# Kernel tuning notes

Measured on AMD Instinct MI355X. Metric: run time of the kernel, lower is better.

The kernel has to match this reference:

```python
import jax, jax.numpy as jnp
import numpy as np

K = 8
HID = 32
BOUND = 5.0
SIGMA_MIN = 1e-4
MIN_DERIV = 1e-3
B, T, C = 32, 4096, 512


def setup_inputs() -> dict:
    key = jax.random.key(0)
    k1, k2, k3 = jax.random.split(key, 3)
    x = jax.random.normal(k1, (B, T, C), jnp.float32)
    W1 = jax.random.normal(k2, (HID, 2), jnp.float32) * 0.5
    b1 = jnp.zeros((HID,), jnp.float32)
    W2 = jax.random.normal(k3, (3 * K + 1, HID), jnp.float32) * 0.1
    b2 = jnp.zeros((3 * K + 1,), jnp.float32)
    return {"x": x, "W1": W1, "b1": b1, "W2": W2, "b2": b2}


def _rqs_forward(x2d, kx, ky, d):
    # x2d: (BC, T); kx, ky, d: (BC, K+1)
    w = kx[:, 1:] - kx[:, :-1]
    h = ky[:, 1:] - ky[:, :-1]
    s = h / jnp.maximum(w, 1e-8)
    idx = jax.vmap(lambda a, v: jnp.searchsorted(a, v, side='right'))(kx, x2d) - 1
    idx = jnp.clip(idx, 0, K - 1)  # (BC, T)
    g = lambda t, i: jnp.take_along_axis(t, i, axis=1)
    w_k = g(w, idx)
    h_k = g(h, idx)
    s_k = g(s, idx)
    d_k = g(d, idx)
    d_k1 = g(d, jnp.minimum(idx + 1, K))
    kx_l = g(kx, idx)
    ky_l = g(ky, idx)
    zeta = jnp.clip((x2d - kx_l) / jnp.maximum(w_k, 1e-8), 0.0, 1.0)
    numer = h_k * (s_k * zeta * zeta + d_k * zeta * (1.0 - zeta))
    denom = s_k + (d_k1 + d_k - 2.0 * s_k) * zeta * (1.0 - zeta)
    z2d = ky_l + numer / jnp.maximum(denom, 1e-8)
    tail = (x2d < -BOUND) | (x2d > BOUND)
    return jnp.where(tail, x2d, z2d)


def reference(x, W1, b1, W2, b2):
    Bb, Tt, Cc = x.shape
    # affine standardisation (unbiased std matching torch.std default)
    mu = jnp.mean(x, axis=1, keepdims=True)
    sig = jnp.maximum(jnp.std(x, axis=1, ddof=1, keepdims=True), SIGMA_MIN)
    z_pre = (x - mu) / sig  # (B, T, C)
    zd = jax.lax.stop_gradient(z_pre)
    skew = jnp.mean(zd ** 3, axis=1)          # (B, C)
    ekurt = jnp.mean(zd ** 4, axis=1) - 3.0   # (B, C)
    stats = jnp.stack([skew, ekurt], axis=-1).reshape(Bb * Cc, 2)
    hid = jax.nn.relu(stats @ W1.T + b1)
    raw = hid @ W2.T + b2                      # (BC, 3K+1)
    widths = jax.nn.softmax(raw[:, :K], axis=-1) * (2.0 * BOUND)
    heights = jax.nn.softmax(raw[:, K:2 * K], axis=-1) * (2.0 * BOUND)
    derivs = jax.nn.softplus(raw[:, 2 * K:]) + MIN_DERIV  # (BC, K+1)
    pad = jnp.full((widths.shape[0], 1), -BOUND, widths.dtype)
    kx = jnp.concatenate([pad, -BOUND + jnp.cumsum(widths, axis=-1)], axis=-1)
    ky = jnp.concatenate([pad, -BOUND + jnp.cumsum(heights, axis=-1)], axis=-1)
    x2d = jnp.transpose(z_pre, (0, 2, 1)).reshape(Bb * Cc, Tt)
    z2d = _rqs_forward(x2d, kx, ky, derivs)
    return jnp.transpose(z2d.reshape(Bb, Cc, Tt), (0, 2, 1))
```

## Files before the change

kernel.cpp:

```cpp
#include <hip/hip_runtime.h>
#include <math.h>

#define KNOTS 8
#define HIDN 32
#define TT 4096
#define CC 512
#define NB 32
#define BOUNDF 5.0f
#define CT 32
#define NTG 16
#define TPT (TT / NTG)
#define NPAIR (TPT / 2)

__global__ __launch_bounds__(512, 2)
void k_fused(const float* __restrict__ x, const float* __restrict__ W1,
             const float* __restrict__ b1, const float* __restrict__ W2,
             const float* __restrict__ b2, float* __restrict__ out)
{
    const int bb = blockIdx.y;
    const int c0 = blockIdx.x * CT;
    const int ci = threadIdx.x & (CT - 1);
    const int tg = threadIdx.x >> 5;

    __shared__ float red[NTG][4][CT];
    __shared__ float mom[4][CT];
    __shared__ float pA[CT], pB[CT];
    __shared__ float pKx[7][CT];
    __shared__ float2 bZ[KNOTS][CT];
    __shared__ float2 bY[KNOTS][CT];
    __shared__ float2 bD[KNOTS][CT];

    const size_t base = (size_t)bb * TT * CC + c0 + ci;
    const float* pxt = x + base + (size_t)tg * CC;

    unsigned int xp[NPAIR];
    float s1 = 0.f, s2 = 0.f, s3 = 0.f, s4 = 0.f;
    #pragma unroll
    for (int m = 0; m < NPAIR; ++m) {
        const float v0 = pxt[(size_t)(2*m)     * (NTG * CC)];
        const float v1 = pxt[(size_t)(2*m + 1) * (NTG * CC)];
        const float v0sq = v0 * v0, v1sq = v1 * v1;
        s1 += v0;                    s1 += v1;
        s2 = fmaf(v0,   v0,   s2);   s2 = fmaf(v1,   v1,   s2);
        s3 = fmaf(v0sq, v0,   s3);   s3 = fmaf(v1sq, v1,   s3);
        s4 = fmaf(v0sq, v0sq, s4);   s4 = fmaf(v1sq, v1sq, s4);
        unsigned int pk;
        asm("v_cvt_pk_bf16_f32 %0, %1, %2" : "=v"(pk) : "v"(v0), "v"(v1));
        xp[m] = pk;
    }
    red[tg][0][ci] = s1; red[tg][1][ci] = s2;
    red[tg][2][ci] = s3; red[tg][3][ci] = s4;
    __syncthreads();

    if (threadIdx.x < 4 * CT) {
        const int m = threadIdx.x >> 5, c = threadIdx.x & (CT - 1);
        float acc = 0.f;
        #pragma unroll
        for (int g = 0; g < NTG; ++g) acc += red[g][m][c];
        mom[m][c] = acc;
    }
    __syncthreads();

    if (threadIdx.x < CT) {
        const int c = threadIdx.x;
        const float n  = (float)TT;
        const float t1 = mom[0][c], t2 = mom[1][c], t3 = mom[2][c], t4 = mom[3][c];
        const float mu  = t1 / n;
        const float ex2 = t2 / n, ex3 = t3 / n, ex4 = t4 / n;
        float var = (t2 - n * mu * mu) / (n - 1.f);
        var = fmaxf(var, 0.f);
        const float sig  = fmaxf(sqrtf(var), 1e-4f);
        const float inv  = 1.f / sig;
        const float mu2  = mu * mu;
        const float ez3  = ex3 - 3.f * mu * ex2 + 2.f * mu * mu2;
        const float ez4  = ex4 - 4.f * mu * ex3 + 6.f * mu2 * ex2 - 3.f * mu2 * mu2;
        const float inv2 = inv * inv;
        const float skew  = ez3 * inv2 * inv;
        const float ekurt = ez4 * inv2 * inv2 - 3.f;

        float hid[HIDN];
        #pragma unroll
        for (int h = 0; h < HIDN; ++h) {
            float v = fmaf(W1[2*h], skew, fmaf(W1[2*h+1], ekurt, b1[h]));
            hid[h] = fmaxf(v, 0.f);
        }

        float e[KNOTS], kxr[KNOTS+1], kyr[KNOTS+1], dr[KNOTS+1];
        {
            float mx = -1e30f;
            #pragma unroll
            for (int o = 0; o < KNOTS; ++o) {
                float acc = b2[o];
                #pragma unroll
                for (int h = 0; h < HIDN; ++h) acc = fmaf(W2[o*HIDN + h], hid[h], acc);
                e[o] = acc; mx = fmaxf(mx, acc);
            }
            float sum = 0.f;
            #pragma unroll
            for (int o = 0; o < KNOTS; ++o) { e[o] = expf(e[o] - mx); sum += e[o]; }
            const float scale = (2.f * BOUNDF) / sum;
            float cum = -BOUNDF; kxr[0] = -BOUNDF;
            #pragma unroll
            for (int o = 0; o < KNOTS; ++o) { cum = fmaf(e[o], scale, cum); kxr[o+1] = cum; }
        }
        {
            float mx = -1e30f;
            #pragma unroll
            for (int o = 0; o < KNOTS; ++o) {
                float acc = b2[KNOTS + o];
                #pragma unroll
                for (int h = 0; h < HIDN; ++h) acc = fmaf(W2[(KNOTS+o)*HIDN + h], hid[h], acc);
                e[o] = acc; mx = fmaxf(mx, acc);
            }
            float sum = 0.f;
            #pragma unroll
            for (int o = 0; o < KNOTS; ++o) { e[o] = expf(e[o] - mx); sum += e[o]; }
            const float scale = (2.f * BOUNDF) / sum;
            float cum = -BOUNDF; kyr[0] = -BOUNDF;
            #pragma unroll
            for (int o = 0; o < KNOTS; ++o) { cum = fmaf(e[o], scale, cum); kyr[o+1] = cum; }
        }
        #pragma unroll
        for (int o = 0; o < KNOTS+1; ++o) {
            float acc = b2[2*KNOTS + o];
            #pragma unroll
            for (int h = 0; h < HIDN; ++h) acc = fmaf(W2[(2*KNOTS+o)*HIDN + h], hid[h], acc);
            float sp = fmaxf(acc, 0.f) + log1pf(expf(-fabsf(acc)));
            dr[o] = sp + 1e-3f;
        }

        pA[c] = inv;
        pB[c] = -mu * inv;
        #pragma unroll
        for (int j = 1; j <= 7; ++j) pKx[j-1][c] = kxr[j];
        #pragma unroll
        for (int j = 0; j < KNOTS; ++j) {
            const float w    = kxr[j+1] - kxr[j];
            const float wm   = fmaxf(w, 1e-8f);
            const float invw = 1.f / wm;
            const float h    = kyr[j+1] - kyr[j];
            bZ[j][c] = make_float2(-kxr[j] * invw, invw);
            bY[j][c] = make_float2(kyr[j], h);
            bD[j][c] = make_float2(dr[j], dr[j] + dr[j+1]);
        }
    }
    __syncthreads();

    const float a  = pA[ci];
    const float bz = pB[ci];
    const float kx1 = pKx[0][ci], kx2 = pKx[1][ci], kx3 = pKx[2][ci],
                kx4 = pKx[3][ci], kx5 = pKx[4][ci], kx6 = pKx[5][ci],
                kx7 = pKx[6][ci];
    float* pot = out + base + (size_t)tg * CC;

    #pragma unroll
    for (int m = 0; m < NPAIR; ++m) {
        const unsigned int u = xp[m];
        const float xv0 = __uint_as_float(u << 16);
        const float xv1 = __uint_as_float(u & 0xffff0000u);
        #pragma unroll
        for (int j = 0; j < 2; ++j) {
            const float xv = (j == 0) ? xv0 : xv1;
            const float z = fmaf(xv, a, bz);
            const bool  c4 = z >= kx4;
            const float mB = c4 ? kx6 : kx2;
            const bool  cB = z >= mB;
            const float nLo = c4 ? kx5 : kx1;
            const float nHi = c4 ? kx7 : kx3;
            const float mC = cB ? nHi : nLo;
            const bool  cC = z >= mC;
            const int off = (c4 ? 4*CT : 0) + (cB ? 2*CT : 0) + (cC ? CT : 0) + ci;

            const float2 Z = ((const float2*)bZ)[off];
            const float2 Y = ((const float2*)bY)[off];
            const float2 D = ((const float2*)bD)[off];

            const float zeta = fmaf(z, Z.y, Z.x);
            const float uu   = fmaf(-zeta, zeta, zeta);
            const float s    = Y.y * Z.y;
            const float R    = fmaf(-2.f, s, D.y);
            const float den  = fmaf(R, uu, s);
            const float inner= fmaf(s * zeta, zeta, D.x * uu);
            const float res  = fmaf(Y.y * inner,
                                    __builtin_amdgcn_rcpf(fmaxf(den, 1e-8f)), Y.x);
            const float o = (fabsf(z) > BOUNDF) ? z : res;
            __builtin_nontemporal_store(o, &pot[(size_t)(2*m + j) * (NTG * CC)]);
        }
    }
}

extern "C" void kernel_launch(void* const* d_in, const int* in_sizes, int n_in,
                              void* d_out, int out_size, void* d_ws, size_t ws_size,
                              hipStream_t stream) {
    const float* x  = (const float*)d_in[0];
    const float* W1 = (const float*)d_in[1];
    const float* b1 = (const float*)d_in[2];
    const float* W2 = (const float*)d_in[3];
    const float* b2 = (const float*)d_in[4];
    float* out = (float*)d_out;

    k_fused<<<dim3(CC / CT, NB), dim3(512), 0, stream>>>(x, W1, b1, W2, b2, out);
}
```

Before: 121.2 us.

## Cache only half the column in registers, re-read the rest to double occupancy

Each thread now keeps only 128 of its 256 timesteps packed as bf16 in registers, down from all 256. The remaining timesteps are streamed once for the moment sums and then re-read from global memory in reverse order during the transform pass, so the most recently loaded data is likely still in cache. Fewer registers allow the launch bound to rise to 4 blocks per SM, which should improve latency hiding. The cost is reading about half of the input a second time, plus extra loop overhead.

```diff
diff --git a/kernel.cpp b/kernel.cpp
--- a/kernel.cpp
+++ b/kernel.cpp
@@ -10,9 +10,9 @@
 #define CT 32
 #define NTG 16
 #define TPT (TT / NTG)
-#define NPAIR (TPT / 2)
-
-__global__ __launch_bounds__(512, 2)
+#define NHOLD 64
+
+__global__ __launch_bounds__(512, 4)
 void k_fused(const float* __restrict__ x, const float* __restrict__ W1,
              const float* __restrict__ b1, const float* __restrict__ W2,
              const float* __restrict__ b2, float* __restrict__ out)
@@ -33,10 +33,10 @@
     const size_t base = (size_t)bb * TT * CC + c0 + ci;
     const float* pxt = x + base + (size_t)tg * CC;
 
-    unsigned int xp[NPAIR];
+    unsigned int xp[NHOLD];
     float s1 = 0.f, s2 = 0.f, s3 = 0.f, s4 = 0.f;
     #pragma unroll
-    for (int m = 0; m < NPAIR; ++m) {
+    for (int m = 0; m < NHOLD; ++m) {
         const float v0 = pxt[(size_t)(2*m)     * (NTG * CC)];
         const float v1 = pxt[(size_t)(2*m + 1) * (NTG * CC)];
         const float v0sq = v0 * v0, v1sq = v1 * v1;
@@ -47,6 +47,15 @@
         unsigned int pk;
         asm("v_cvt_pk_bf16_f32 %0, %1, %2" : "=v"(pk) : "v"(v0), "v"(v1));
         xp[m] = pk;
+    }
+    #pragma unroll 8
+    for (int k = 2 * NHOLD; k < TPT; ++k) {
+        const float v  = pxt[(size_t)k * (NTG * CC)];
+        const float v2 = v * v;
+        s1 += v;
+        s2 = fmaf(v,  v,  s2);
+        s3 = fmaf(v2, v,  s3);
+        s4 = fmaf(v2, v2, s4);
     }
     red[tg][0][ci] = s1; red[tg][1][ci] = s2;
     red[tg][2][ci] = s3; red[tg][3][ci] = s4;
@@ -153,8 +162,40 @@
                 kx7 = pKx[6][ci];
     float* pot = out + base + (size_t)tg * CC;
 
+    for (int kb = TPT / 8 - 1; kb >= 2 * NHOLD / 8; --kb) {
+        float xv[8];
+        #pragma unroll
+        for (int j = 0; j < 8; ++j)
+            xv[j] = pxt[(size_t)(kb * 8 + j) * (NTG * CC)];
+        #pragma unroll
+        for (int j = 0; j < 8; ++j) {
+            const float z = fmaf(xv[j], a, bz);
+            const bool  c4 = z >= kx4;
+            const float mB = c4 ? kx6 : kx2;
+            const bool  cB = z >= mB;
+            const float nLo = c4 ? kx5 : kx1;
+            const float nHi = c4 ? kx7 : kx3;
+            const float mC = cB ? nHi : nLo;
+            const bool  cC = z >= mC;
+            const int off = (c4 ? 4*CT : 0) + (cB ? 2*CT : 0) + (cC ? CT : 0) + ci;
+            const float2 Z = ((const float2*)bZ)[off];
+            const float2 Y = ((const float2*)bY)[off];
+            const float2 D = ((const float2*)bD)[off];
+            const float zeta = fmaf(z, Z.y, Z.x);
+            const float uu   = fmaf(-zeta, zeta, zeta);
+            const float s    = Y.y * Z.y;
+            const float R    = fmaf(-2.f, s, D.y);
+            const float den  = fmaf(R, uu, s);
+            const float inner= fmaf(s * zeta, zeta, D.x * uu);
+            const float res  = fmaf(Y.y * inner,
+                                    __builtin_amdgcn_rcpf(fmaxf(den, 1e-8f)), Y.x);
+            const float o = (fabsf(z) > BOUNDF) ? z : res;
+            __builtin_nontemporal_store(o, &pot[(size_t)(kb * 8 + j) * (NTG * CC)]);
+        }
+    }
+
     #pragma unroll
-    for (int m = 0; m < NPAIR; ++m) {
+    for (int m = 0; m < NHOLD; ++m) {
         const unsigned int u = xp[m];
         const float xv0 = __uint_as_float(u << 16);
         const float xv1 = __uint_as_float(u & 0xffff0000u);
@@ -170,11 +211,9 @@
             const float mC = cB ? nHi : nLo;
             const bool  cC = z >= mC;
             const int off = (c4 ? 4*CT : 0) + (cB ? 2*CT : 0) + (cC ? CT : 0) + ci;
-
             const float2 Z = ((const float2*)bZ)[off];
             const float2 Y = ((const float2*)bY)[off];
             const float2 D = ((const float2*)bD)[off];
-
             const float zeta = fmaf(z, Z.y, Z.x);
             const float uu   = fmaf(-zeta, zeta, zeta);
             const float s    = Y.y * Z.y;
```

Result: no change. 120.8 us (-0.3%).

## Stream input through double-buffered LDS via async global_load_lds

Applied to the files above, without the earlier changes.

Replaces direct per-thread global loads in the moment-accumulation pass with async global-to-LDS loads into a double-buffered staging area. Each wave issues 16 rows per chunk, waits on vmcnt, and reads values back from LDS while the next chunk is in flight. This aims to keep more memory requests outstanding and cut register pressure from the fully unrolled loads. In exchange it adds 64KB of LDS, which may limit occupancy to fewer than two blocks per CU, and relies on hand-placed waitcnt ordering.

```diff
diff --git a/kernel.cpp b/kernel.cpp
--- a/kernel.cpp
+++ b/kernel.cpp
@@ -11,6 +11,11 @@
 #define NTG 16
 #define TPT (TT / NTG)
 #define NPAIR (TPT / 2)
+#define CH 16
+#define NBUF (TPT / CH)
+
+typedef __attribute__((address_space(3))) void       lds_void;
+typedef const __attribute__((address_space(1))) void g_void;
 
 __global__ __launch_bounds__(512, 2)
 void k_fused(const float* __restrict__ x, const float* __restrict__ W1,
@@ -21,7 +26,10 @@
     const int c0 = blockIdx.x * CT;
     const int ci = threadIdx.x & (CT - 1);
     const int tg = threadIdx.x >> 5;
-
+    const int w  = threadIdx.x >> 6;
+    const int ln = threadIdx.x & 63;
+
+    __shared__ float stage[2][8][CH * 64];
     __shared__ float red[NTG][4][CT];
     __shared__ float mom[4][CT];
     __shared__ float pA[CT], pB[CT];
@@ -35,19 +43,44 @@
 
     unsigned int xp[NPAIR];
     float s1 = 0.f, s2 = 0.f, s3 = 0.f, s4 = 0.f;
+
+#define ISSUE(BUF, KBASE)                                                        \
+    {                                                                            \
+        float* dst_ = &stage[(BUF)][w][0];                                       \
+        _Pragma("unroll")                                                        \
+        for (int r_ = 0; r_ < CH; ++r_)                                          \
+            __builtin_amdgcn_global_load_lds(                                    \
+                (g_void*)(pxt + (size_t)((KBASE) + r_) * (NTG * CC)),            \
+                (lds_void*)(dst_ + r_ * 64), 4, 0, 0);                           \
+    }
+
+    ISSUE(0, 0);
     #pragma unroll
-    for (int m = 0; m < NPAIR; ++m) {
-        const float v0 = pxt[(size_t)(2*m)     * (NTG * CC)];
-        const float v1 = pxt[(size_t)(2*m + 1) * (NTG * CC)];
-        const float v0sq = v0 * v0, v1sq = v1 * v1;
-        s1 += v0;                    s1 += v1;
-        s2 = fmaf(v0,   v0,   s2);   s2 = fmaf(v1,   v1,   s2);
-        s3 = fmaf(v0sq, v0,   s3);   s3 = fmaf(v1sq, v1,   s3);
-        s4 = fmaf(v0sq, v0sq, s4);   s4 = fmaf(v1sq, v1sq, s4);
-        unsigned int pk;
-        asm("v_cvt_pk_bf16_f32 %0, %1, %2" : "=v"(pk) : "v"(v0), "v"(v1));
-        xp[m] = pk;
-    }
+    for (int blk = 0; blk < NBUF; ++blk) {
+        if (blk + 1 < NBUF) {
+            asm volatile("s_waitcnt lgkmcnt(0)" ::: "memory");
+            ISSUE((blk + 1) & 1, (blk + 1) * CH);
+            asm volatile("s_waitcnt vmcnt(16)" ::: "memory");
+        } else {
+            asm volatile("s_waitcnt vmcnt(0)" ::: "memory");
+        }
+        const float* src = &stage[blk & 1][w][0];
+        #pragma unroll
+        for (int p = 0; p < CH / 2; ++p) {
+            const float v0 = src[(2 * p)     * 64 + ln];
+            const float v1 = src[(2 * p + 1) * 64 + ln];
+            const float v0sq = v0 * v0, v1sq = v1 * v1;
+            s1 += v0;                    s1 += v1;
+            s2 = fmaf(v0,   v0,   s2);   s2 = fmaf(v1,   v1,   s2);
+            s3 = fmaf(v0sq, v0,   s3);   s3 = fmaf(v1sq, v1,   s3);
+            s4 = fmaf(v0sq, v0sq, s4);   s4 = fmaf(v1sq, v1sq, s4);
+            unsigned int pk;
+            asm("v_cvt_pk_bf16_f32 %0, %1, %2" : "=v"(pk) : "v"(v0), "v"(v1));
+            xp[blk * (CH / 2) + p] = pk;
+        }
+    }
+#undef ISSUE
+
     red[tg][0][ci] = s1; red[tg][1][ci] = s2;
     red[tg][2][ci] = s3; red[tg][3][ci] = s4;
     __syncthreads();
@@ -135,8 +168,8 @@
         for (int j = 1; j <= 7; ++j) pKx[j-1][c] = kxr[j];
         #pragma unroll
         for (int j = 0; j < KNOTS; ++j) {
-            const float w    = kxr[j+1] - kxr[j];
-            const float wm   = fmaxf(w, 1e-8f);
+            const float w_    = kxr[j+1] - kxr[j];
+            const float wm   = fmaxf(w_, 1e-8f);
             const float invw = 1.f / wm;
             const float h    = kyr[j+1] - kyr[j];
             bZ[j][c] = make_float2(-kxr[j] * invw, invw);
```

Result: slower. 125.6 us (+3.6%).

## Vectorize loads/stores to float4 per thread with channel-major per-thread layout

Applied to the files above, without the earlier changes.

Each thread now handles 4 adjacent channels using 16-byte vector loads and nontemporal vector stores, with 64 time groups of 8 lanes instead of 16 groups of 32 lanes. Moment accumulation and spline evaluation are done per channel lane, and the spline tables are re-laid out as [q][knot][padded col] for bank-conflict-free lookup. The aim is fewer memory instructions and wider transactions in a bandwidth-bound kernel. In exchange, register use rises (four sets of knot thresholds and moments per thread) and each warp covers only 8 rows of 128 bytes per access, which may hurt coalescing.

```diff
diff --git a/kernel.cpp b/kernel.cpp
--- a/kernel.cpp
+++ b/kernel.cpp
@@ -8,9 +8,12 @@
 #define NB 32
 #define BOUNDF 5.0f
 #define CT 32
-#define NTG 16
-#define TPT (TT / NTG)
-#define NPAIR (TPT / 2)
+#define NTG 64
+#define NLD 64
+#define NPAIR 128
+#define TPAD 9
+
+typedef float f32x4 __attribute__((ext_vector_type(4)));
 
 __global__ __launch_bounds__(512, 2)
 void k_fused(const float* __restrict__ x, const float* __restrict__ W1,
@@ -19,37 +22,47 @@
 {
     const int bb = blockIdx.y;
     const int c0 = blockIdx.x * CT;
-    const int ci = threadIdx.x & (CT - 1);
-    const int tg = threadIdx.x >> 5;
+    const int lc = threadIdx.x & 7;
+    const int tg = threadIdx.x >> 3;
 
     __shared__ float red[NTG][4][CT];
     __shared__ float mom[4][CT];
     __shared__ float pA[CT], pB[CT];
     __shared__ float pKx[7][CT];
-    __shared__ float2 bZ[KNOTS][CT];
-    __shared__ float2 bY[KNOTS][CT];
-    __shared__ float2 bD[KNOTS][CT];
-
-    const size_t base = (size_t)bb * TT * CC + c0 + ci;
-    const float* pxt = x + base + (size_t)tg * CC;
+    __shared__ float2 bZ4[4][KNOTS][TPAD];
+    __shared__ float2 bY4[4][KNOTS][TPAD];
+    __shared__ float2 bD4[4][KNOTS][TPAD];
+
+    const size_t base = (size_t)bb * TT * CC + c0 + 4 * lc + (size_t)tg * CC;
+    const f32x4* pxt = (const f32x4*)(x + base);
 
     unsigned int xp[NPAIR];
-    float s1 = 0.f, s2 = 0.f, s3 = 0.f, s4 = 0.f;
-    #pragma unroll
-    for (int m = 0; m < NPAIR; ++m) {
-        const float v0 = pxt[(size_t)(2*m)     * (NTG * CC)];
-        const float v1 = pxt[(size_t)(2*m + 1) * (NTG * CC)];
-        const float v0sq = v0 * v0, v1sq = v1 * v1;
-        s1 += v0;                    s1 += v1;
-        s2 = fmaf(v0,   v0,   s2);   s2 = fmaf(v1,   v1,   s2);
-        s3 = fmaf(v0sq, v0,   s3);   s3 = fmaf(v1sq, v1,   s3);
-        s4 = fmaf(v0sq, v0sq, s4);   s4 = fmaf(v1sq, v1sq, s4);
-        unsigned int pk;
-        asm("v_cvt_pk_bf16_f32 %0, %1, %2" : "=v"(pk) : "v"(v0), "v"(v1));
-        xp[m] = pk;
-    }
-    red[tg][0][ci] = s1; red[tg][1][ci] = s2;
-    red[tg][2][ci] = s3; red[tg][3][ci] = s4;
+    float s1[4] = {0,0,0,0}, s2[4] = {0,0,0,0}, s3[4] = {0,0,0,0}, s4[4] = {0,0,0,0};
+    #pragma unroll
+    for (int k = 0; k < NLD; ++k) {
+        const f32x4 v = pxt[(size_t)k * (NTG * CC / 4)];
+        #pragma unroll
+        for (int q = 0; q < 4; ++q) {
+            const float vv = v[q];
+            const float v2 = vv * vv;
+            s1[q] += vv;
+            s2[q] = fmaf(vv, vv, s2[q]);
+            s3[q] = fmaf(v2, vv, s3[q]);
+            s4[q] = fmaf(v2, v2, s4[q]);
+        }
+        unsigned int pk0, pk1;
+        asm("v_cvt_pk_bf16_f32 %0, %1, %2" : "=v"(pk0) : "v"(v[0]), "v"(v[1]));
+        asm("v_cvt_pk_bf16_f32 %0, %1, %2" : "=v"(pk1) : "v"(v[2]), "v"(v[3]));
+        xp[2*k]   = pk0;
+        xp[2*k+1] = pk1;
+    }
+    #pragma unroll
+    for (int q = 0; q < 4; ++q) {
+        red[tg][0][4*lc+q] = s1[q];
+        red[tg][1][4*lc+q] = s2[q];
+        red[tg][2][4*lc+q] = s3[q];
+        red[tg][3][4*lc+q] = s4[q];
+    }
     __syncthreads();
 
     if (threadIdx.x < 4 * CT) {
@@ -133,47 +146,55 @@
         pB[c] = -mu * inv;
         #pragma unroll
         for (int j = 1; j <= 7; ++j) pKx[j-1][c] = kxr[j];
+        const int q = c & 3, cc = c >> 2;
         #pragma unroll
         for (int j = 0; j < KNOTS; ++j) {
             const float w    = kxr[j+1] - kxr[j];
             const float wm   = fmaxf(w, 1e-8f);
             const float invw = 1.f / wm;
             const float h    = kyr[j+1] - kyr[j];
-            bZ[j][c] = make_float2(-kxr[j] * invw, invw);
-            bY[j][c] = make_float2(kyr[j], h);
-            bD[j][c] = make_float2(dr[j], dr[j] + dr[j+1]);
+            bZ4[q][j][cc] = make_float2(-kxr[j] * invw, invw);
+            bY4[q][j][cc] = make_float2(kyr[j], h);
+            bD4[q][j][cc] = make_float2(dr[j], dr[j] + dr[j+1]);
         }
     }
     __syncthreads();
 
-    const float a  = pA[ci];
-    const float bz = pB[ci];
-    const float kx1 = pKx[0][ci], kx2 = pKx[1][ci], kx3 = pKx[2][ci],
-                kx4 = pKx[3][ci], kx5 = pKx[4][ci], kx6 = pKx[5][ci],
-                kx7 = pKx[6][ci];
-    float* pot = out + base + (size_t)tg * CC;
-
-    #pragma unroll
-    for (int m = 0; m < NPAIR; ++m) {
-        const unsigned int u = xp[m];
-        const float xv0 = __uint_as_float(u << 16);
-        const float xv1 = __uint_as_float(u & 0xffff0000u);
-        #pragma unroll
-        for (int j = 0; j < 2; ++j) {
-            const float xv = (j == 0) ? xv0 : xv1;
-            const float z = fmaf(xv, a, bz);
-            const bool  c4 = z >= kx4;
-            const float mB = c4 ? kx6 : kx2;
+    float aq[4], bq[4], kx[4][7];
+    #pragma unroll
+    for (int q = 0; q < 4; ++q) {
+        const int c = 4*lc + q;
+        aq[q] = pA[c];
+        bq[q] = pB[c];
+        #pragma unroll
+        for (int j = 0; j < 7; ++j) kx[q][j] = pKx[j][c];
+    }
+    f32x4* pot = (f32x4*)(out + base);
+
+    #pragma unroll
+    for (int k = 0; k < NLD; ++k) {
+        const unsigned int u0 = xp[2*k], u1 = xp[2*k+1];
+        float xv[4];
+        xv[0] = __uint_as_float(u0 << 16);
+        xv[1] = __uint_as_float(u0 & 0xffff0000u);
+        xv[2] = __uint_as_float(u1 << 16);
+        xv[3] = __uint_as_float(u1 & 0xffff0000u);
+        f32x4 r;
+        #pragma unroll
+        for (int q = 0; q < 4; ++q) {
+            const float z = fmaf(xv[q], aq[q], bq[q]);
+            const bool  c4 = z >= kx[q][3];
+            const float mB = c4 ? kx[q][5] : kx[q][1];
             const bool  cB = z >= mB;
-            const float nLo = c4 ? kx5 : kx1;
-            const float nHi = c4 ? kx7 : kx3;
+            const float nLo = c4 ? kx[q][4] : kx[q][0];
+            const float nHi = c4 ? kx[q][6] : kx[q][2];
             const float mC = cB ? nHi : nLo;
             const bool  cC = z >= mC;
-            const int off = (c4 ? 4*CT : 0) + (cB ? 2*CT : 0) + (cC ? CT : 0) + ci;
-
-            const float2 Z = ((const float2*)bZ)[off];
-            const float2 Y = ((const float2*)bY)[off];
-            const float2 D = ((const float2*)bD)[off];
+            const int idx = (c4 ? 4 : 0) + (cB ? 2 : 0) + (cC ? 1 : 0);
+
+            const float2 Z = bZ4[q][idx][lc];
+            const float2 Y = bY4[q][idx][lc];
+            const float2 D = bD4[q][idx][lc];
 
             const float zeta = fmaf(z, Z.y, Z.x);
             const float uu   = fmaf(-zeta, zeta, zeta);
@@ -183,9 +204,9 @@
             const float inner= fmaf(s * zeta, zeta, D.x * uu);
             const float res  = fmaf(Y.y * inner,
                                     __builtin_amdgcn_rcpf(fmaxf(den, 1e-8f)), Y.x);
-            const float o = (fabsf(z) > BOUNDF) ? z : res;
-            __builtin_nontemporal_store(o, &pot[(size_t)(2*m + j) * (NTG * CC)]);
-        }
+            r[q] = (fabsf(z) > BOUNDF) ? z : res;
+        }
+        __builtin_nontemporal_store(r, &pot[(size_t)k * (NTG * CC / 4)]);
     }
 }
 
```

New measurement: 120.2 us. No clear change (-0.8%).
